# Performance work log

Hardware: AMD Instinct MI355X
Metric: run time of the kernel (lower is better)

The kernel has to match this reference:

```python
import jax, jax.numpy as jnp
import numpy as np

B, S, D = 8, 1024, 768
H, DK = 12, 64
DFF = 3072
EPS = 1e-5


def setup_inputs() -> dict:
    key = jax.random.key(0)
    ks = jax.random.split(key, 12)
    s = lambda fan_in: 1.0 / np.sqrt(fan_in)
    return {
        "x": jax.random.normal(ks[0], (B, S, D), jnp.float32),
        "Wq": jax.random.normal(ks[1], (D, D), jnp.float32) * s(D),
        "Wk": jax.random.normal(ks[2], (D, D), jnp.float32) * s(D),
        "Wv": jax.random.normal(ks[3], (D, D), jnp.float32) * s(D),
        "Wo": jax.random.normal(ks[4], (D, D), jnp.float32) * s(D),
        "g1": jnp.ones((D,), jnp.float32),
        "b1": jnp.zeros((D,), jnp.float32),
        "g2": jnp.ones((D,), jnp.float32),
        "b2": jnp.zeros((D,), jnp.float32),
        "W1": jax.random.normal(ks[5], (D, DFF), jnp.float32) * s(D),
        "bW1": jnp.zeros((DFF,), jnp.float32),
        "W2": jax.random.normal(ks[6], (DFF, D), jnp.float32) * s(DFF),
        "bW2": jnp.zeros((D,), jnp.float32),
    }


def _layernorm(x, g, b):
    mu = x.mean(-1, keepdims=True)
    var = ((x - mu) ** 2).mean(-1, keepdims=True)
    return (x - mu) * jax.lax.rsqrt(var + EPS) * g + b


def reference(x, Wq, Wk, Wv, Wo, g1, b1, g2, b2, W1, bW1, W2, bW2):
    scale = DK ** (-0.5)
    # pre-norm attention block
    h = _layernorm(x, g1, b1)
    q = (h @ Wq).reshape(B, S, H, DK)
    k = (h @ Wk).reshape(B, S, H, DK)
    v = (h @ Wv).reshape(B, S, H, DK)
    logits = jnp.einsum("bqhd,bkhd->bhqk", q, k) * scale  # [B,H,S,S]
    weights = jax.nn.softmax(logits, axis=-1)
    attn = jnp.einsum("bhqk,bkhd->bqhd", weights, v).reshape(B, S, D)
    x = x + attn @ Wo
    # pre-norm FFN block
    h = _layernorm(x, g2, b2)
    h = jax.nn.gelu(h @ W1 + bW1, approximate=False)
    x = x + h @ W2 + bW2
    return x
```

## Files before the change

kernel.cpp:

```cpp
#include <hip/hip_runtime.h>
#include <cstdint>
#include <cstddef>

#define B_   8
#define S_   1024
#define D_   768
#define H_   12
#define DK_  64
#define DFF_ 3072
#define M_   (B_*S_)

typedef __attribute__((ext_vector_type(8))) short  short8;
typedef __attribute__((ext_vector_type(4))) short  short4v;
typedef __attribute__((ext_vector_type(8))) __bf16 bf16x8;
typedef __attribute__((ext_vector_type(4))) float  f32x4;
typedef __attribute__((ext_vector_type(4))) unsigned uint4v;
typedef __attribute__((ext_vector_type(2))) unsigned uint2v;

__device__ __forceinline__ unsigned short f2bf(float f) {
    unsigned u = __builtin_bit_cast(unsigned, f);
    u += 0x7FFFu + ((u >> 16) & 1u);
    return (unsigned short)(u >> 16);
}

__device__ __forceinline__ unsigned pkbf(float a, float b) {
    unsigned short ua = __builtin_bit_cast(unsigned short, (__bf16)a);
    unsigned short ub = __builtin_bit_cast(unsigned short, (__bf16)b);
    return (unsigned)ua | ((unsigned)ub << 16);
}

__device__ __forceinline__ f32x4 mfma16(short8 a, short8 b, f32x4 c) {
    return __builtin_amdgcn_mfma_f32_16x16x32_bf16(
        __builtin_bit_cast(bf16x8, a), __builtin_bit_cast(bf16x8, b), c, 0, 0, 0);
}

__device__ __forceinline__ void gload16(const void* g, void* l) {
    auto gp = reinterpret_cast<const __attribute__((address_space(1))) unsigned*>(
        reinterpret_cast<uintptr_t>(g));
    auto lp = reinterpret_cast<__attribute__((address_space(3))) unsigned*>(
        reinterpret_cast<uintptr_t>(l));
    __builtin_amdgcn_global_load_lds(gp, lp, 16, 0, 0);
}

__device__ __forceinline__ float gelu_f(float v) {
    return 0.5f * v * (1.0f + erff(v * 0.70710678118654752f));
}

__global__ __launch_bounds__(256) void wtrans4_kernel(
    const float* __restrict__ W0, const float* __restrict__ W1,
    const float* __restrict__ W2, const float* __restrict__ W3,
    unsigned short* __restrict__ Wt)
{
    __shared__ float tile[32][33];
    int z = blockIdx.z;
    const float* W = (z == 0) ? W0 : (z == 1) ? W1 : (z == 2) ? W2 : W3;
    unsigned short* dst = Wt + (size_t)z * 768 * 768;
    int n0 = blockIdx.x * 32, k0 = blockIdx.y * 32;
    int tx = threadIdx.x, ty = threadIdx.y;
#pragma unroll
    for (int j = 0; j < 4; ++j)
        tile[ty + j*8][tx] = W[(size_t)(k0 + ty + j*8) * 768 + n0 + tx];
    __syncthreads();
#pragma unroll
    for (int j = 0; j < 4; ++j)
        dst[(size_t)(n0 + ty + j*8) * 768 + k0 + tx] = f2bf(tile[tx][ty + j*8]);
}

__global__ __launch_bounds__(256) void wtrans_kernel(
    const float* __restrict__ W, unsigned short* __restrict__ Wt, int K, int N)
{
    __shared__ float tile[32][33];
    int n0 = blockIdx.x * 32, k0 = blockIdx.y * 32;
    int tx = threadIdx.x, ty = threadIdx.y;
#pragma unroll
    for (int j = 0; j < 4; ++j)
        tile[ty + j*8][tx] = W[(size_t)(k0 + ty + j*8) * N + n0 + tx];
    __syncthreads();
#pragma unroll
    for (int j = 0; j < 4; ++j)
        Wt[(size_t)(n0 + ty + j*8) * K + k0 + tx] = f2bf(tile[tx][ty + j*8]);
}

__global__ __launch_bounds__(256) void ln_kernel(
    const float* __restrict__ x, const float* __restrict__ g,
    const float* __restrict__ b, unsigned short* __restrict__ out)
{
    int row = blockIdx.x, t = threadIdx.x;
    const float* xr = x + (size_t)row * D_;
    float v[3];
#pragma unroll
    for (int i = 0; i < 3; ++i) v[i] = xr[t + i*256];
    float s  = v[0] + v[1] + v[2];
    float ss = v[0]*v[0] + v[1]*v[1] + v[2]*v[2];
#pragma unroll
    for (int d = 1; d < 64; d <<= 1) { s += __shfl_xor(s, d); ss += __shfl_xor(ss, d); }
    __shared__ float red[8];
    int w = t >> 6, lane = t & 63;
    if (lane == 0) { red[w] = s; red[4 + w] = ss; }
    __syncthreads();
    s  = red[0] + red[1] + red[2] + red[3];
    ss = red[4] + red[5] + red[6] + red[7];
    float mu   = s * (1.0f / D_);
    float var  = ss * (1.0f / D_) - mu * mu;
    float rstd = rsqrtf(var + 1e-5f);
    unsigned short* orow = out + (size_t)row * D_;
#pragma unroll
    for (int i = 0; i < 3; ++i) {
        int c = t + i*256;
        orow[c] = f2bf((v[i] - mu) * rstd * g[c] + b[c]);
    }
}

template<int BN, int EPI>
__global__ __launch_bounds__(256, 2) void gemm_kernel(
    const unsigned short* __restrict__ A, const unsigned short* __restrict__ Wt,
    const float* __restrict__ bias, const float* __restrict__ resid,
    void* __restrict__ outp, int N, int K)
{
    __shared__ unsigned short Al[2][128*64];
    __shared__ unsigned short Bl[2][BN*64];
    constexpr int NJ = BN / 64;
    const int nbn = N / BN;
    const int nwg = gridDim.x;
    const int p = blockIdx.x;
    const int bid = (p & 7) * (nwg >> 3) + (p >> 3);
    const int bm = bid / nbn, bn = bid % nbn;
    const int t = threadIdx.x;
    const int lane = t & 63, w = t >> 6;
    const int wm = w >> 1, wn = w & 1;
    const int lr = lane & 15, lh = lane >> 4;
    const char* aBase = (const char*)(A  + (size_t)(bm*128) * K);
    const char* bBase = (const char*)(Wt + (size_t)(bn*BN)  * K);

    f32x4 acc[4][2*NJ] = {};

    auto stage = [&](int kt, int buf) {
        const int k0b = kt << 7;
#pragma unroll
        for (int shot = 0; shot < 4; ++shot) {
            int d = shot*4096 + t*16;
            int row = d >> 7;
            int ch  = ((d >> 4) & 7) ^ (row & 7);
            gload16(aBase + (size_t)row*(K*2) + k0b + ch*16, (char*)&Al[buf][0] + d);
        }
#pragma unroll
        for (int shot = 0; shot < 2*NJ; ++shot) {
            int d = shot*4096 + t*16;
            int row = d >> 7;
            int ch  = ((d >> 4) & 7) ^ (row & 7);
            gload16(bBase + (size_t)row*(K*2) + k0b + ch*16, (char*)&Bl[buf][0] + d);
        }
    };

    const int nk = K >> 6;
    stage(0, 0);
    stage(1, 1);

    for (int it = 0; it < nk; ++it) {
        const int buf = it & 1;
        if (it + 1 < nk) {
            if constexpr (BN == 128) asm volatile("s_waitcnt vmcnt(8)" ::: "memory");
            else                     asm volatile("s_waitcnt vmcnt(6)" ::: "memory");
        } else {
            asm volatile("s_waitcnt vmcnt(0)" ::: "memory");
        }
        __builtin_amdgcn_s_barrier();

        short8 af[2][4], bf[2][2*NJ];
#pragma unroll
        for (int kk = 0; kk < 2; ++kk) {
#pragma unroll
            for (int i = 0; i < 4; ++i)
                af[kk][i] = *reinterpret_cast<const short8*>(
                    &Al[buf][(wm*64 + i*16 + lr)*64 + (((kk*4 + lh) ^ (lr & 7))*8)]);
#pragma unroll
            for (int j = 0; j < 2*NJ; ++j)
                bf[kk][j] = *reinterpret_cast<const short8*>(
                    &Bl[buf][(wn*(32*NJ) + j*16 + lr)*64 + (((kk*4 + lh) ^ (lr & 7))*8)]);
        }
        __builtin_amdgcn_s_setprio(1);
#pragma unroll
        for (int kk = 0; kk < 2; ++kk)
#pragma unroll
            for (int i = 0; i < 4; ++i)
#pragma unroll
                for (int j = 0; j < 2*NJ; ++j)
                    acc[i][j] = mfma16(af[kk][i], bf[kk][j], acc[i][j]);
        __builtin_amdgcn_s_setprio(0);
        __builtin_amdgcn_s_barrier();
        if (it + 2 < nk) stage(it + 2, buf);
    }

#pragma unroll
    for (int i = 0; i < 4; ++i) {
#pragma unroll
        for (int r = 0; r < 4; ++r) {
            int row = bm*128 + wm*64 + i*16 + lh*4 + r;
#pragma unroll
            for (int j = 0; j < 2*NJ; ++j) {
                int col = bn*BN + wn*(32*NJ) + j*16 + lr;
                float v = acc[i][j][r];
                if (EPI == 0) {
                    ((unsigned short*)outp)[(size_t)row*N + col] = f2bf(v);
                } else if (EPI == 1) {
                    v += bias[col];
                    v = gelu_f(v);
                    ((unsigned short*)outp)[(size_t)row*N + col] = f2bf(v);
                } else {
                    if (bias) v += bias[col];
                    v += resid[(size_t)row*N + col];
                    ((float*)outp)[(size_t)row*N + col] = v;
                }
            }
        }
    }
}

__global__ __launch_bounds__(256) void vtrans_kernel(
    const unsigned short* __restrict__ qkv, unsigned short* __restrict__ vt)
{
    __shared__ unsigned short tl[64][65];
    int bid = blockIdx.x;
    int sblk = bid & 15, bh = bid >> 4;
    int b = bh / H_, h = bh % H_;
    int t = threadIdx.x, tx = t & 63, ty = t >> 6;
    int s0 = sblk * 64;
#pragma unroll
    for (int j = 0; j < 16; ++j) {
        int s = j*4 + ty;
        tl[s][tx] = qkv[(size_t)(b*S_ + s0 + s)*2304 + 1536 + h*64 + tx];
    }
    __syncthreads();
#pragma unroll
    for (int j = 0; j < 16; ++j) {
        int dk = j*4 + ty;
        vt[((size_t)bh*64 + dk)*S_ + s0 + tx] = tl[tx][dk];
    }
}

__global__ __launch_bounds__(256, 3) void attn_kernel(
    const unsigned short* __restrict__ qkv, const unsigned short* __restrict__ vt,
    unsigned short* __restrict__ out)
{
    __shared__ unsigned short Kl[2][64*64];
    __shared__ unsigned short Vl[2][64*64];

    const int p = blockIdx.x;
    const int l = (p & 7) * 96 + (p >> 3);
    const int qb = l & 7, bh = l >> 3;
    const int b = bh / H_, h = bh % H_;
    const int t = threadIdx.x, lane = t & 63, w = t >> 6;
    const int lr = lane & 15, lh = lane >> 4;
    const int sz = (lr & 7) << 3;

    const float SC = 0.125f * 1.44269504089f;

    const int qrow0 = qb*128 + w*32;
    short8 bq[2][2];
#pragma unroll
    for (int qi = 0; qi < 2; ++qi) {
        const unsigned short* qp = qkv + (size_t)(b*S_ + qrow0 + qi*16 + lr)*2304 + h*64;
#pragma unroll
        for (int c = 0; c < 2; ++c)
            bq[qi][c] = *reinterpret_cast<const short8*>(&qp[c*32 + lh*8]);
    }

    float m_run[2] = {-1e30f, -1e30f};
    float l_run[2] = {0.f, 0.f};
    f32x4 o[2][4] = {};

    const char* kgbase = (const char*)qkv;
    const char* vgbase = (const char*)vt;

    auto stage = [&](int kb, int buf) {
        const int ks = kb * 64;
#pragma unroll
        for (int shot = 0; shot < 2; ++shot) {
            int d = shot*4096 + t*16;
            int row = d >> 7;
            int colb = d & 127;
            int sc = colb ^ ((row & 7) << 4);
            const char* ksrc = kgbase + ((size_t)(b*S_ + ks + row)*2304 + 768 + h*64)*2 + sc;
            gload16(ksrc, (char*)&Kl[buf][0] + d);
            const char* vsrc = vgbase + ((size_t)(bh*64 + row)*1024 + ks)*2 + sc;
            gload16(vsrc, (char*)&Vl[buf][0] + d);
        }
    };

    stage(0, 0);
    asm volatile("s_waitcnt vmcnt(0)" ::: "memory");
    __builtin_amdgcn_s_barrier();

    for (int kb = 0; kb < 16; ++kb) {
        const int buf = kb & 1;
        if (kb < 15) stage(kb + 1, buf ^ 1);

        short8 ak[4][2];
#pragma unroll
        for (int j = 0; j < 4; ++j)
#pragma unroll
            for (int c = 0; c < 2; ++c)
                ak[j][c] = *reinterpret_cast<const short8*>(
                    &Kl[buf][(j*16 + lr)*64 + ((c*32 + lh*8) ^ sz)]);

        short8 av[4][2];
#pragma unroll
        for (int j = 0; j < 4; ++j) {
            const unsigned short* vrow = &Vl[buf][(j*16 + lr)*64];
#pragma unroll
            for (int ks = 0; ks < 2; ++ks) {
                short4v lo = *reinterpret_cast<const short4v*>(&vrow[(ks*32 + lh*4)      ^ sz]);
                short4v hi = *reinterpret_cast<const short4v*>(&vrow[(ks*32 + 16 + lh*4) ^ sz]);
                av[j][ks] = __builtin_shufflevector(lo, hi, 0,1,2,3,4,5,6,7);
            }
        }

#pragma unroll
        for (int qi = 0; qi < 2; ++qi) {
            f32x4 s[4];
            __builtin_amdgcn_s_setprio(1);
#pragma unroll
            for (int j = 0; j < 4; ++j) {
                f32x4 z = {0.f, 0.f, 0.f, 0.f};
                z = mfma16(ak[j][0], bq[qi][0], z);
                z = mfma16(ak[j][1], bq[qi][1], z);
                s[j] = z;
            }
            __builtin_amdgcn_s_setprio(0);

            float m01 = fmaxf(fmaxf(s[0][0], s[0][1]), fmaxf(s[0][2], s[0][3]));
            float m1  = fmaxf(fmaxf(s[1][0], s[1][1]), fmaxf(s[1][2], s[1][3]));
            float m2  = fmaxf(fmaxf(s[2][0], s[2][1]), fmaxf(s[2][2], s[2][3]));
            float m3  = fmaxf(fmaxf(s[3][0], s[3][1]), fmaxf(s[3][2], s[3][3]));
            float mt = fmaxf(fmaxf(m01, m1), fmaxf(m2, m3)) * SC;
            mt = fmaxf(mt, __shfl_xor(mt, 16));
            mt = fmaxf(mt, __shfl_xor(mt, 32));

            if (__any(mt > m_run[qi] + 8.0f)) {
                float mn = fmaxf(m_run[qi], mt);
                float a  = exp2f(m_run[qi] - mn);
                m_run[qi] = mn;
                l_run[qi] *= a;
#pragma unroll
                for (int j = 0; j < 4; ++j)
#pragma unroll
                    for (int r = 0; r < 4; ++r) o[qi][j][r] *= a;
            }

            const float negm = -m_run[qi];
            float rs = 0.f;
#pragma unroll
            for (int j = 0; j < 4; ++j)
#pragma unroll
                for (int r = 0; r < 4; ++r) {
                    float pv = exp2f(__builtin_fmaf(s[j][r], SC, negm));
                    s[j][r] = pv;
                    rs += pv;
                }
            l_run[qi] += rs;

            uint4v u0 = { pkbf(s[0][0], s[0][1]), pkbf(s[0][2], s[0][3]),
                          pkbf(s[1][0], s[1][1]), pkbf(s[1][2], s[1][3]) };
            uint4v u1 = { pkbf(s[2][0], s[2][1]), pkbf(s[2][2], s[2][3]),
                          pkbf(s[3][0], s[3][1]), pkbf(s[3][2], s[3][3]) };
            short8 pb0 = __builtin_bit_cast(short8, u0);
            short8 pb1 = __builtin_bit_cast(short8, u1);

            __builtin_amdgcn_s_setprio(1);
#pragma unroll
            for (int j = 0; j < 4; ++j) {
                o[qi][j] = mfma16(av[j][0], pb0, o[qi][j]);
                o[qi][j] = mfma16(av[j][1], pb1, o[qi][j]);
            }
            __builtin_amdgcn_s_setprio(0);
        }

        asm volatile("s_waitcnt vmcnt(0)" ::: "memory");
        __builtin_amdgcn_s_barrier();
    }

#pragma unroll
    for (int qi = 0; qi < 2; ++qi) {
        float ls = l_run[qi];
        ls += __shfl_xor(ls, 16);
        ls += __shfl_xor(ls, 32);
        float inv = 1.0f / ls;
        int q = qrow0 + qi*16 + lr;
        unsigned short* orow = out + (size_t)(b*S_ + q)*D_ + h*64;
#pragma unroll
        for (int j = 0; j < 4; ++j) {
            uint2v vv = { pkbf(o[qi][j][0]*inv, o[qi][j][1]*inv),
                          pkbf(o[qi][j][2]*inv, o[qi][j][3]*inv) };
            *reinterpret_cast<uint2v*>(&orow[j*16 + lh*4]) = vv;
        }
    }
}

extern "C" void kernel_launch(void* const* d_in, const int* in_sizes, int n_in,
                              void* d_out, int out_size, void* d_ws, size_t ws_size,
                              hipStream_t stream)
{
    (void)in_sizes; (void)n_in; (void)out_size; (void)ws_size;
    const float* x   = (const float*)d_in[0];
    const float* Wq  = (const float*)d_in[1];
    const float* Wk  = (const float*)d_in[2];
    const float* Wv  = (const float*)d_in[3];
    const float* Wo  = (const float*)d_in[4];
    const float* g1  = (const float*)d_in[5];
    const float* b1  = (const float*)d_in[6];
    const float* g2  = (const float*)d_in[7];
    const float* b2  = (const float*)d_in[8];
    const float* W1  = (const float*)d_in[9];
    const float* bW1 = (const float*)d_in[10];
    const float* W2  = (const float*)d_in[11];
    const float* bW2 = (const float*)d_in[12];
    float* out = (float*)d_out;

    char* ws = (char*)d_ws;
    unsigned short* wt_qkv = (unsigned short*)(ws);
    unsigned short* wt_o   = (unsigned short*)(ws + 3538944);
    unsigned short* wt_1   = (unsigned short*)(ws + 4718592);
    unsigned short* wt_2   = (unsigned short*)(ws + 9437184);
    unsigned short* slotA  = (unsigned short*)(ws + 14155776);
    unsigned short* qkv    = (unsigned short*)(ws + 26738688);
    unsigned short* vt     = (unsigned short*)(ws + 64487424);
    unsigned short* ffm    = qkv;

    dim3 tb(32, 8);
    wtrans4_kernel<<<dim3(24,24,4), tb, 0, stream>>>(Wq, Wk, Wv, Wo, wt_qkv);
    wtrans_kernel<<<dim3(96,24), tb, 0, stream>>>(W1, wt_1, 768, 3072);
    wtrans_kernel<<<dim3(24,96), tb, 0, stream>>>(W2, wt_2, 3072, 768);

    ln_kernel<<<M_, 256, 0, stream>>>(x, g1, b1, slotA);
    gemm_kernel<128,0><<<64*18, 256, 0, stream>>>(slotA, wt_qkv, nullptr, nullptr, qkv, 2304, 768);
    vtrans_kernel<<<1536, 256, 0, stream>>>(qkv, vt);
    attn_kernel<<<768, 256, 0, stream>>>(qkv, vt, slotA);
    gemm_kernel<64,2><<<64*12, 256, 0, stream>>>(slotA, wt_o, nullptr, x, (void*)out, 768, 768);
    ln_kernel<<<M_, 256, 0, stream>>>(out, g2, b2, slotA);
    gemm_kernel<128,1><<<64*24, 256, 0, stream>>>(slotA, wt_1, bW1, nullptr, ffm, 3072, 768);
    gemm_kernel<64,2><<<64*12, 256, 0, stream>>>(ffm, wt_2, bW2, out, (void*)out, 768, 3072);
}
```

Measured before the change: 305.9 us.

## Swap MFMA operands for vectorized epilogue, tanh-GELU, precomputed load addresses

The GEMM now swaps the A/B operands of the MFMA so that each lane holds four consecutive output columns of one row. The epilogue can then do 16-byte float and 8-byte packed bf16 stores and vectorized bias/residual loads instead of scalar ones. The exact erf GELU is replaced with a tanh-style sigmoid approximation using hardware exp2 and reciprocal, which changes numerics slightly. Global-to-LDS load addresses are precomputed once per thread so the staging loop only adds a k offset.

```diff
diff --git a/kernel.cpp b/kernel.cpp
--- a/kernel.cpp
+++ b/kernel.cpp
@@ -42,8 +42,10 @@
     __builtin_amdgcn_global_load_lds(gp, lp, 16, 0, 0);
 }
 
-__device__ __forceinline__ float gelu_f(float v) {
-    return 0.5f * v * (1.0f + erff(v * 0.70710678118654752f));
+__device__ __forceinline__ float gelu_fast(float v) {
+    float w = v * __builtin_fmaf(v * v, 0.044715f, 1.0f);
+    float e = __builtin_amdgcn_exp2f(-2.3021178f * w);
+    return v * __builtin_amdgcn_rcpf(1.0f + e);
 }
 
 __global__ __launch_bounds__(256) void wtrans4_kernel(
@@ -120,6 +122,7 @@
     __shared__ unsigned short Al[2][128*64];
     __shared__ unsigned short Bl[2][BN*64];
     constexpr int NJ = BN / 64;
+    constexpr int ASH = 4, BSH = 2*NJ;
     const int nbn = N / BN;
     const int nwg = gridDim.x;
     const int p = blockIdx.x;
@@ -132,24 +135,32 @@
     const char* aBase = (const char*)(A  + (size_t)(bm*128) * K);
     const char* bBase = (const char*)(Wt + (size_t)(bn*BN)  * K);
 
+    uintptr_t aAdr[ASH], bAdr[BSH];
+#pragma unroll
+    for (int s = 0; s < ASH; ++s) {
+        int d = s*4096 + t*16;
+        int row = d >> 7;
+        int ch  = ((d >> 4) & 7) ^ (row & 7);
+        aAdr[s] = (uintptr_t)aBase + (size_t)row*(K*2) + ch*16;
+    }
+#pragma unroll
+    for (int s = 0; s < BSH; ++s) {
+        int d = s*4096 + t*16;
+        int row = d >> 7;
+        int ch  = ((d >> 4) & 7) ^ (row & 7);
+        bAdr[s] = (uintptr_t)bBase + (size_t)row*(K*2) + ch*16;
+    }
+
     f32x4 acc[4][2*NJ] = {};
 
     auto stage = [&](int kt, int buf) {
         const int k0b = kt << 7;
 #pragma unroll
-        for (int shot = 0; shot < 4; ++shot) {
-            int d = shot*4096 + t*16;
-            int row = d >> 7;
-            int ch  = ((d >> 4) & 7) ^ (row & 7);
-            gload16(aBase + (size_t)row*(K*2) + k0b + ch*16, (char*)&Al[buf][0] + d);
-        }
-#pragma unroll
-        for (int shot = 0; shot < 2*NJ; ++shot) {
-            int d = shot*4096 + t*16;
-            int row = d >> 7;
-            int ch  = ((d >> 4) & 7) ^ (row & 7);
-            gload16(bBase + (size_t)row*(K*2) + k0b + ch*16, (char*)&Bl[buf][0] + d);
-        }
+        for (int s = 0; s < ASH; ++s)
+            gload16((const void*)(aAdr[s] + k0b), (char*)&Al[buf][0] + s*4096 + t*16);
+#pragma unroll
+        for (int s = 0; s < BSH; ++s)
+            gload16((const void*)(bAdr[s] + k0b), (char*)&Bl[buf][0] + s*4096 + t*16);
     };
 
     const int nk = K >> 6;
@@ -166,16 +177,16 @@
         }
         __builtin_amdgcn_s_barrier();
 
-        short8 af[2][4], bf[2][2*NJ];
+        short8 xf[2][4], wf[2][2*NJ];
 #pragma unroll
         for (int kk = 0; kk < 2; ++kk) {
 #pragma unroll
             for (int i = 0; i < 4; ++i)
-                af[kk][i] = *reinterpret_cast<const short8*>(
+                xf[kk][i] = *reinterpret_cast<const short8*>(
                     &Al[buf][(wm*64 + i*16 + lr)*64 + (((kk*4 + lh) ^ (lr & 7))*8)]);
 #pragma unroll
             for (int j = 0; j < 2*NJ; ++j)
-                bf[kk][j] = *reinterpret_cast<const short8*>(
+                wf[kk][j] = *reinterpret_cast<const short8*>(
                     &Bl[buf][(wn*(32*NJ) + j*16 + lr)*64 + (((kk*4 + lh) ^ (lr & 7))*8)]);
         }
         __builtin_amdgcn_s_setprio(1);
@@ -185,7 +196,7 @@
             for (int i = 0; i < 4; ++i)
 #pragma unroll
                 for (int j = 0; j < 2*NJ; ++j)
-                    acc[i][j] = mfma16(af[kk][i], bf[kk][j], acc[i][j]);
+                    acc[i][j] = mfma16(wf[kk][j], xf[kk][i], acc[i][j]);
         __builtin_amdgcn_s_setprio(0);
         __builtin_amdgcn_s_barrier();
         if (it + 2 < nk) stage(it + 2, buf);
@@ -193,24 +204,24 @@
 
 #pragma unroll
     for (int i = 0; i < 4; ++i) {
-#pragma unroll
-        for (int r = 0; r < 4; ++r) {
-            int row = bm*128 + wm*64 + i*16 + lh*4 + r;
-#pragma unroll
-            for (int j = 0; j < 2*NJ; ++j) {
-                int col = bn*BN + wn*(32*NJ) + j*16 + lr;
-                float v = acc[i][j][r];
-                if (EPI == 0) {
-                    ((unsigned short*)outp)[(size_t)row*N + col] = f2bf(v);
-                } else if (EPI == 1) {
-                    v += bias[col];
-                    v = gelu_f(v);
-                    ((unsigned short*)outp)[(size_t)row*N + col] = f2bf(v);
-                } else {
-                    if (bias) v += bias[col];
-                    v += resid[(size_t)row*N + col];
-                    ((float*)outp)[(size_t)row*N + col] = v;
-                }
+        const int m = bm*128 + wm*64 + i*16 + lr;
+#pragma unroll
+        for (int j = 0; j < 2*NJ; ++j) {
+            const int n0 = bn*BN + wn*(32*NJ) + j*16 + lh*4;
+            f32x4 v = acc[i][j];
+            if (EPI == 1) {
+                f32x4 bb = *reinterpret_cast<const f32x4*>(&bias[n0]);
+                v += bb;
+#pragma unroll
+                for (int r = 0; r < 4; ++r) v[r] = gelu_fast(v[r]);
+            }
+            if (EPI == 2) {
+                if (bias) v += *reinterpret_cast<const f32x4*>(&bias[n0]);
+                v += *reinterpret_cast<const f32x4*>(&resid[(size_t)m*N + n0]);
+                *reinterpret_cast<f32x4*>(&((float*)outp)[(size_t)m*N + n0]) = v;
+            } else {
+                uint2v pv = { pkbf(v[0], v[1]), pkbf(v[2], v[3]) };
+                *reinterpret_cast<uint2v*>(&((unsigned short*)outp)[(size_t)m*N + n0]) = pv;
             }
         }
     }
@@ -432,11 +443,11 @@
     wtrans_kernel<<<dim3(24,96), tb, 0, stream>>>(W2, wt_2, 3072, 768);
 
     ln_kernel<<<M_, 256, 0, stream>>>(x, g1, b1, slotA);
-    gemm_kernel<128,0><<<64*18, 256, 0, stream>>>(slotA, wt_qkv, nullptr, nullptr, qkv, 2304, 768);
+    gemm_kernel<128,0><<<1152, 256, 0, stream>>>(slotA, wt_qkv, nullptr, nullptr, qkv, 2304, 768);
     vtrans_kernel<<<1536, 256, 0, stream>>>(qkv, vt);
     attn_kernel<<<768, 256, 0, stream>>>(qkv, vt, slotA);
-    gemm_kernel<64,2><<<64*12, 256, 0, stream>>>(slotA, wt_o, nullptr, x, (void*)out, 768, 768);
+    gemm_kernel<64,2><<<768, 256, 0, stream>>>(slotA, wt_o, nullptr, x, (void*)out, 768, 768);
     ln_kernel<<<M_, 256, 0, stream>>>(out, g2, b2, slotA);
-    gemm_kernel<128,1><<<64*24, 256, 0, stream>>>(slotA, wt_1, bW1, nullptr, ffm, 3072, 768);
-    gemm_kernel<64,2><<<64*12, 256, 0, stream>>>(ffm, wt_2, bW2, out, (void*)out, 768, 3072);
-}
+    gemm_kernel<128,1><<<1536, 256, 0, stream>>>(slotA, wt_1, bW1, nullptr, ffm, 3072, 768);
+    gemm_kernel<64,2><<<768, 256, 0, stream>>>(ffm, wt_2, bW2, out, (void*)out, 768, 3072);
+}
```

After: 283.1 us. 7.4% less time.
